# Optimization experiments

Hardware: AMD Instinct MI355X
Metric: run time of the kernel (lower is better)

## Reference

```python
import jax, jax.numpy as jnp
import numpy as np

B, S, H = 2, 2048, 4096
NH, NKV, HD = 32, 8, 128
Q_SIZE, KV_SIZE = NH * HD, NKV * HD
ROPE_THETA = 10000.0


def setup_inputs() -> dict:
    key = jax.random.key(0)
    k1, k2, k3 = jax.random.split(key, 3)
    positions = jnp.tile(jnp.arange(S, dtype=jnp.int64 if jax.config.jax_enable_x64 else jnp.int32), (B, 1))
    hidden_states = jax.random.normal(k1, (B, S, H), dtype=jnp.float32)
    w_qkv = jax.random.normal(k2, (H, Q_SIZE + 2 * KV_SIZE), dtype=jnp.float32) * 0.02
    w_o = jax.random.normal(k3, (Q_SIZE, H), dtype=jnp.float32) * 0.02
    return {"positions": positions, "hidden_states": hidden_states, "w_qkv": w_qkv, "w_o": w_o}


def _apply_rope(x, positions):
    # x: [B, S, nheads, HD]; neox-style rotate-half RoPE
    half = HD // 2
    inv_freq = 1.0 / (ROPE_THETA ** (jnp.arange(0, half, dtype=jnp.float32) / half))
    freqs = positions.astype(jnp.float32)[..., None] * inv_freq  # [B, S, HD/2]
    cos = jnp.cos(freqs)[:, :, None, :]  # [B, S, 1, HD/2]
    sin = jnp.sin(freqs)[:, :, None, :]
    x1, x2 = x[..., :half], x[..., half:]
    return jnp.concatenate([x1 * cos - x2 * sin, x2 * cos + x1 * sin], axis=-1)


def reference(positions, hidden_states, w_qkv, w_o):
    qkv = jnp.einsum("bsh,hd->bsd", hidden_states, w_qkv)
    q = qkv[..., :Q_SIZE].reshape(B, S, NH, HD)
    k = qkv[..., Q_SIZE:Q_SIZE + KV_SIZE].reshape(B, S, NKV, HD)
    v = qkv[..., Q_SIZE + KV_SIZE:].reshape(B, S, NKV, HD)

    q = _apply_rope(q, positions)
    k = _apply_rope(k, positions)

    # GQA: expand kv heads to match query heads
    rep = NH // NKV
    k = jnp.repeat(k, rep, axis=2)  # [B, S, NH, HD]
    v = jnp.repeat(v, rep, axis=2)

    scale = 1.0 / jnp.sqrt(jnp.float32(HD))
    scores = jnp.einsum("bqhd,bkhd->bhqk", q, k) * scale  # [B, NH, S, S]
    causal = jnp.tril(jnp.ones((S, S), dtype=bool))
    scores = jnp.where(causal[None, None], scores, jnp.finfo(scores.dtype).min)
    probs = jax.nn.softmax(scores, axis=-1)

    attn = jnp.einsum("bhqk,bkhd->bqhd", probs, v).reshape(B, S, Q_SIZE)
    return jnp.einsum("bsd,dh->bsh", attn, w_o)
```

## Files before the change

### kernel.cpp

```cpp
#include <hip/hip_runtime.h>
#include <hip/hip_bf16.h>
#include <math.h>


typedef __attribute__((ext_vector_type(8))) __bf16 bf16x8;
typedef __attribute__((ext_vector_type(4))) float floatx4;

__device__ __forceinline__ floatx4 mfma16(bf16x8 a, bf16x8 b, floatx4 c) {
    return __builtin_amdgcn_mfma_f32_16x16x32_bf16(a, b, c, 0, 0, 0);
}

__device__ __forceinline__ void load_lds16(const __hip_bfloat16* g,
                                           __hip_bfloat16* lds_base_uniform) {
    __builtin_amdgcn_global_load_lds(
        (const __attribute__((address_space(1))) unsigned int*)g,
        (__attribute__((address_space(3))) unsigned int*)lds_base_uniform,
        16, 0, 0);
}

__global__ __launch_bounds__(256)
void convert_kernel(const float* __restrict__ in, __hip_bfloat16* __restrict__ out,
                    int n) {
    int i = (blockIdx.x * 256 + threadIdx.x) * 4;
    if (i >= n) return;
    float4 v = *(const float4*)(in + i);
    union { __hip_bfloat16 h[4]; uint2 u; } pk;
    pk.h[0] = __float2bfloat16(v.x);
    pk.h[1] = __float2bfloat16(v.y);
    pk.h[2] = __float2bfloat16(v.z);
    pk.h[3] = __float2bfloat16(v.w);
    *(uint2*)(out + i) = pk.u;
}

__global__ __launch_bounds__(256)
void transpose_f32_bf16_kernel(const float* __restrict__ in,
                               __hip_bfloat16* __restrict__ out, int R, int C) {
    __shared__ __hip_bfloat16 tile[64][65];
    const int r0 = blockIdx.y * 64, c0 = blockIdx.x * 64;
    const int t = threadIdx.x;
    #pragma unroll
    for (int i = 0; i < 16; ++i) {
        int idx = t + 256 * i;
        int rl = idx >> 6, cl = idx & 63;
        tile[rl][cl] = __float2bfloat16(in[(size_t)(r0 + rl) * C + (c0 + cl)]);
    }
    __syncthreads();
    #pragma unroll
    for (int i = 0; i < 16; ++i) {
        int idx = t + 256 * i;
        int cl = idx >> 6, rl = idx & 63;
        out[(size_t)(c0 + cl) * R + (r0 + rl)] = tile[rl][cl];
    }
}

__global__ __launch_bounds__(256)
void transpose_bf16_kernel(const __hip_bfloat16* __restrict__ in,
                           __hip_bfloat16* __restrict__ out, int R, int C) {
    __shared__ __hip_bfloat16 tile[64][65];
    const int bz = blockIdx.z;
    const __hip_bfloat16* inb  = in  + (size_t)bz * R * C;
    __hip_bfloat16*       outb = out + (size_t)bz * R * C;
    const int r0 = blockIdx.y * 64, c0 = blockIdx.x * 64;
    const int t = threadIdx.x;
    #pragma unroll
    for (int i = 0; i < 16; ++i) {
        int idx = t + 256 * i;
        int rl = idx >> 6, cl = idx & 63;
        tile[rl][cl] = inb[(size_t)(r0 + rl) * C + (c0 + cl)];
    }
    __syncthreads();
    #pragma unroll
    for (int i = 0; i < 16; ++i) {
        int idx = t + 256 * i;
        int cl = idx >> 6, rl = idx & 63;
        outb[(size_t)(c0 + cl) * R + (r0 + rl)] = tile[rl][cl];
    }
}

template <int MODE>
__global__ __launch_bounds__(256)
void gemm_bt_kernel(const __hip_bfloat16* __restrict__ A,
                    const __hip_bfloat16* __restrict__ Bt,
                    float* __restrict__ Cp,
                    __hip_bfloat16* __restrict__ Qr,
                    __hip_bfloat16* __restrict__ Kr,
                    __hip_bfloat16* __restrict__ Vv,
                    int M, int N, int K) {
    __shared__ __align__(16) __hip_bfloat16 As[128 * 32];
    __shared__ __align__(16) __hip_bfloat16 Bs[128 * 32];

    const int m0 = blockIdx.y * 128, n0 = blockIdx.x * 128;
    const int tid  = threadIdx.x;
    const int wave = tid >> 6, lane = tid & 63;
    const int quad = lane >> 4, l16 = lane & 15;
    const int wm = (wave >> 1) * 64, wn = (wave & 1) * 64;

    floatx4 acc[4][4] = {};

    for (int kt = 0; kt < K; kt += 32) {
        #pragma unroll
        for (int i = 0; i < 2; ++i) {
            int idx = tid + 256 * i;
            int row = idx >> 2;
            int kc  = (idx & 3) << 3;
            __hip_bfloat16* dstA = &As[(size_t)(wave * 64 + 256 * i) * 8];
            __hip_bfloat16* dstB = &Bs[(size_t)(wave * 64 + 256 * i) * 8];
            load_lds16(&A [(size_t)(m0 + row) * K + kt + kc], dstA);
            load_lds16(&Bt[(size_t)(n0 + row) * K + kt + kc], dstB);
        }
        __syncthreads();

        bf16x8 af[4], bfv[4];
        #pragma unroll
        for (int i = 0; i < 4; ++i)
            af[i]  = *(const bf16x8*)(&As[(wm + i * 16 + l16) * 32 + quad * 8]);
        #pragma unroll
        for (int j = 0; j < 4; ++j)
            bfv[j] = *(const bf16x8*)(&Bs[(wn + j * 16 + l16) * 32 + quad * 8]);
        #pragma unroll
        for (int i = 0; i < 4; ++i)
            #pragma unroll
            for (int j = 0; j < 4; ++j)
                acc[i][j] = mfma16(af[i], bfv[j], acc[i][j]);
        __syncthreads();
    }

    #pragma unroll
    for (int i = 0; i < 4; ++i) {
        #pragma unroll
        for (int j = 0; j < 4; ++j) {
            int col = n0 + wn + j * 16 + l16;
            #pragma unroll
            for (int r = 0; r < 4; ++r) {
                int row = m0 + wm + i * 16 + quad * 4 + r;
                if (MODE == 0) {
                    Cp[(size_t)row * N + col] = acc[i][j][r];
                } else {
                    __hip_bfloat16 v = __float2bfloat16(acc[i][j][r]);
                    int bb = row >> 11, s = row & 2047;
                    int d  = col & 127;
                    if (col < 4096) {
                        int h = col >> 7;
                        Qr[(((size_t)bb * 32 + h) * 2048 + s) * 128 + d] = v;
                    } else if (col < 5120) {
                        int kvh = (col - 4096) >> 7;
                        Kr[(((size_t)bb * 8 + kvh) * 2048 + s) * 128 + d] = v;
                    } else {
                        int kvh = (col - 5120) >> 7;
                        Vv[(((size_t)bb * 8 + kvh) * 2048 + s) * 128 + d] = v;
                    }
                }
            }
        }
    }
}

__global__ __launch_bounds__(256)
void rope_kernel(__hip_bfloat16* __restrict__ x,
                 const int* __restrict__ positions, int nrows, int bshift) {
    int gid = blockIdx.x * 256 + threadIdx.x;
    if (gid >= nrows * 64) return;
    int row = gid >> 6, d = gid & 63;
    int s = row & 2047;
    int b = row >> bshift;
    float p = (float)positions[(b << 11) + s];
    float ang = p * expf(-0.14391156831212787f * (float)d);
    float sn, cs;
    sincosf(ang, &sn, &cs);
    __hip_bfloat16* ptr = x + (size_t)row * 128;
    float x1 = __bfloat162float(ptr[d]);
    float x2 = __bfloat162float(ptr[d + 64]);
    ptr[d]      = __float2bfloat16(x1 * cs - x2 * sn);
    ptr[d + 64] = __float2bfloat16(x2 * cs + x1 * sn);
}

__global__ __launch_bounds__(256)
void attn_kernel(const __hip_bfloat16* __restrict__ Qr,
                 const __hip_bfloat16* __restrict__ Kr,
                 const __hip_bfloat16* __restrict__ Vt,
                 __hip_bfloat16* __restrict__ Ao) {
    __shared__ __align__(16) __hip_bfloat16 Ks[32 * 136];
    __shared__ __align__(16) __hip_bfloat16 Vs[128 * 36];
    __shared__ __align__(16) __hip_bfloat16 Pl[4][32 * 40];

    const int tid  = threadIdx.x;
    const int wave = tid >> 6, lane = tid & 63;
    const int quad = lane >> 4, l16 = lane & 15;
    const int qb = (gridDim.x - 1) - blockIdx.x;
    const int q0 = qb * 128;
    const int qr0 = q0 + wave * 32;
    const int h  = blockIdx.y;
    const int b  = blockIdx.z;
    const int kv = h >> 2;

    const __hip_bfloat16* Qb = Qr + ((size_t)b * 32 + h)  * 2048 * 128;
    const __hip_bfloat16* Kb = Kr + ((size_t)b * 8  + kv) * 2048 * 128;
    const __hip_bfloat16* Vb = Vt + ((size_t)b * 8  + kv) * 128 * 2048;

    bf16x8 qf[2][4];
    #pragma unroll
    for (int i = 0; i < 2; ++i)
        #pragma unroll
        for (int kc = 0; kc < 4; ++kc)
            qf[i][kc] = *(const bf16x8*)(
                &Qb[(size_t)(qr0 + i * 16 + l16) * 128 + kc * 32 + quad * 8]);

    float m_i[2][4], l_i[2][4];
    #pragma unroll
    for (int i = 0; i < 2; ++i)
        #pragma unroll
        for (int r = 0; r < 4; ++r) { m_i[i][r] = -1e30f; l_i[i][r] = 0.0f; }
    floatx4 o[2][8] = {};

    const float scale = 0.08838834764831845f;
    const int kmax = q0 + 127;

    for (int ks = 0; ks <= kmax; ks += 32) {
        #pragma unroll
        for (int p = 0; p < 2; ++p) {
            int idx = tid + 256 * p;
            int krow = idx >> 4, kcol = (idx & 15) << 3;
            *(uint4*)(&Ks[krow * 136 + kcol]) =
                *(const uint4*)(&Kb[(size_t)(ks + krow) * 128 + kcol]);
        }
        #pragma unroll
        for (int p = 0; p < 2; ++p) {
            int idx = tid + 256 * p;
            int d = idx >> 2, koff = (idx & 3) << 3;
            *(uint4*)(&Vs[d * 36 + koff]) =
                *(const uint4*)(&Vb[(size_t)d * 2048 + ks + koff]);
        }
        __syncthreads();

        if (ks <= qr0 + 31) {
            floatx4 sacc[2][2] = {};
            #pragma unroll
            for (int j = 0; j < 2; ++j) {
                #pragma unroll
                for (int kc = 0; kc < 4; ++kc) {
                    bf16x8 kf = *(const bf16x8*)(
                        &Ks[(j * 16 + l16) * 136 + kc * 32 + quad * 8]);
                    #pragma unroll
                    for (int i = 0; i < 2; ++i)
                        sacc[i][j] = mfma16(qf[i][kc], kf, sacc[i][j]);
                }
            }

            float pv[2][2][4], alpha[2][4];
            #pragma unroll
            for (int i = 0; i < 2; ++i) {
                #pragma unroll
                for (int r = 0; r < 4; ++r) {
                    int row = qr0 + i * 16 + quad * 4 + r;
                    float s0 = sacc[i][0][r] * scale;
                    float s1 = sacc[i][1][r] * scale;
                    if (ks + l16 > row)      s0 = -1e30f;
                    if (ks + 16 + l16 > row) s1 = -1e30f;
                    float mx = fmaxf(s0, s1);
                    #pragma unroll
                    for (int off = 1; off < 16; off <<= 1)
                        mx = fmaxf(mx, __shfl_xor(mx, off, 64));
                    float mnew = fmaxf(m_i[i][r], mx);
                    float a  = __expf(m_i[i][r] - mnew);
                    float p0 = __expf(s0 - mnew);
                    float p1 = __expf(s1 - mnew);
                    float rs = p0 + p1;
                    #pragma unroll
                    for (int off = 1; off < 16; off <<= 1)
                        rs += __shfl_xor(rs, off, 64);
                    l_i[i][r] = l_i[i][r] * a + rs;
                    m_i[i][r] = mnew;
                    alpha[i][r] = a;
                    pv[i][0][r] = p0;
                    pv[i][1][r] = p1;
                }
            }

            #pragma unroll
            for (int i = 0; i < 2; ++i)
                #pragma unroll
                for (int dn = 0; dn < 8; ++dn)
                    #pragma unroll
                    for (int r = 0; r < 4; ++r)
                        o[i][dn][r] *= alpha[i][r];

            #pragma unroll
            for (int i = 0; i < 2; ++i)
                #pragma unroll
                for (int j = 0; j < 2; ++j)
                    #pragma unroll
                    for (int r = 0; r < 4; ++r)
                        Pl[wave][(i * 16 + quad * 4 + r) * 40 + j * 16 + l16] =
                            __float2bfloat16(pv[i][j][r]);

            bf16x8 pf[2];
            #pragma unroll
            for (int i = 0; i < 2; ++i)
                pf[i] = *(const bf16x8*)(&Pl[wave][(i * 16 + l16) * 40 + quad * 8]);

            #pragma unroll
            for (int dn = 0; dn < 8; ++dn) {
                bf16x8 vf = *(const bf16x8*)(
                    &Vs[(dn * 16 + l16) * 36 + quad * 8]);
                #pragma unroll
                for (int i = 0; i < 2; ++i)
                    o[i][dn] = mfma16(pf[i], vf, o[i][dn]);
            }
        }
        __syncthreads();
    }

    #pragma unroll
    for (int i = 0; i < 2; ++i) {
        #pragma unroll
        for (int r = 0; r < 4; ++r) {
            float inv = 1.0f / l_i[i][r];
            int row = qr0 + i * 16 + quad * 4 + r;
            size_t base = ((size_t)b * 2048 + row) * 4096 + (size_t)h * 128;
            #pragma unroll
            for (int dn = 0; dn < 8; ++dn)
                Ao[base + dn * 16 + l16] = __float2bfloat16(o[i][dn][r] * inv);
        }
    }
}

extern "C" void kernel_launch(void* const* d_in, const int* in_sizes, int n_in,
                              void* d_out, int out_size, void* d_ws, size_t ws_size,
                              hipStream_t stream) {
    const int*   positions = (const int*)d_in[0];
    const float* hidden    = (const float*)d_in[1];
    const float* wqkv      = (const float*)d_in[2];
    const float* wo        = (const float*)d_in[3];
    float* out = (float*)d_out;

    __hip_bfloat16* WqkvT = (__hip_bfloat16*)d_ws;
    __hip_bfloat16* WoT   = WqkvT + 25165824;
    __hip_bfloat16* Hb    = WoT   + 16777216;
    __hip_bfloat16* Qr    = Hb    + 16777216;
    __hip_bfloat16* Kr    = Qr    + 16777216;
    __hip_bfloat16* Vv    = Kr    + 4194304;
    __hip_bfloat16* Ao    = WqkvT;
    __hip_bfloat16* Vt    = Hb;

    convert_kernel<<<16777216 / 1024, 256, 0, stream>>>(hidden, Hb, 16777216);
    transpose_f32_bf16_kernel<<<dim3(6144 / 64, 4096 / 64), 256, 0, stream>>>(
        wqkv, WqkvT, 4096, 6144);
    transpose_f32_bf16_kernel<<<dim3(4096 / 64, 4096 / 64), 256, 0, stream>>>(
        wo, WoT, 4096, 4096);

    gemm_bt_kernel<1><<<dim3(6144 / 128, 4096 / 128), 256, 0, stream>>>(
        Hb, WqkvT, nullptr, Qr, Kr, Vv, 4096, 6144, 4096);

    rope_kernel<<<(131072 * 64) / 256, 256, 0, stream>>>(Qr, positions, 131072, 16);
    rope_kernel<<<(32768  * 64) / 256, 256, 0, stream>>>(Kr, positions, 32768, 14);

    transpose_bf16_kernel<<<dim3(128 / 64, 2048 / 64, 16), 256, 0, stream>>>(
        Vv, Vt, 2048, 128);

    attn_kernel<<<dim3(2048 / 128, 32, 2), 256, 0, stream>>>(Qr, Kr, Vt, Ao);

    gemm_bt_kernel<0><<<dim3(4096 / 128, 4096 / 128), 256, 0, stream>>>(
        Ao, WoT, out, nullptr, nullptr, nullptr, 4096, 4096, 4096);
}
```

Baseline: 1.222 ms.

## Double KV tile to 64 and prefetch next tile into registers during softmax

The attention kernel now processes 64 keys per iteration instead of 32, which halves the number of barrier-synchronised iterations. It prefetches the next K/V tile from global memory into registers while the current tile's softmax runs, so load latency overlaps compute. It also writes probabilities straight to LDS inside the softmax loop, raises wave priority around the MFMA blocks, and sets a minimum-occupancy launch bound. The trade-off is higher register and LDS use per block, plus more wasted work on partially masked diagonal tiles.

```diff
diff --git a/kernel.cpp b/kernel.cpp
--- a/kernel.cpp
+++ b/kernel.cpp
@@ -174,14 +174,14 @@
     ptr[d + 64] = __float2bfloat16(x2 * cs + x1 * sn);
 }
 
-__global__ __launch_bounds__(256)
+__global__ __launch_bounds__(256, 3)
 void attn_kernel(const __hip_bfloat16* __restrict__ Qr,
                  const __hip_bfloat16* __restrict__ Kr,
                  const __hip_bfloat16* __restrict__ Vt,
                  __hip_bfloat16* __restrict__ Ao) {
-    __shared__ __align__(16) __hip_bfloat16 Ks[32 * 136];
-    __shared__ __align__(16) __hip_bfloat16 Vs[128 * 36];
-    __shared__ __align__(16) __hip_bfloat16 Pl[4][32 * 40];
+    __shared__ __align__(16) __hip_bfloat16 Ks[64 * 132];
+    __shared__ __align__(16) __hip_bfloat16 Vs[128 * 68];
+    __shared__ __align__(16) __hip_bfloat16 Pl[4][32 * 68];
 
     const int tid  = threadIdx.x;
     const int wave = tid >> 6, lane = tid & 63;
@@ -197,6 +197,9 @@
     const __hip_bfloat16* Kb = Kr + ((size_t)b * 8  + kv) * 2048 * 128;
     const __hip_bfloat16* Vb = Vt + ((size_t)b * 8  + kv) * 128 * 2048;
 
+    const int krow = tid >> 4,            kcol = (tid & 15) << 3;
+    const int vrow = tid >> 3,            vcol = (tid & 7)  << 3;
+
     bf16x8 qf[2][4];
     #pragma unroll
     for (int i = 0; i < 2; ++i)
@@ -215,67 +218,88 @@
     const float scale = 0.08838834764831845f;
     const int kmax = q0 + 127;
 
-    for (int ks = 0; ks <= kmax; ks += 32) {
-        #pragma unroll
-        for (int p = 0; p < 2; ++p) {
-            int idx = tid + 256 * p;
-            int krow = idx >> 4, kcol = (idx & 15) << 3;
-            *(uint4*)(&Ks[krow * 136 + kcol]) =
-                *(const uint4*)(&Kb[(size_t)(ks + krow) * 128 + kcol]);
-        }
-        #pragma unroll
-        for (int p = 0; p < 2; ++p) {
-            int idx = tid + 256 * p;
-            int d = idx >> 2, koff = (idx & 3) << 3;
-            *(uint4*)(&Vs[d * 36 + koff]) =
-                *(const uint4*)(&Vb[(size_t)d * 2048 + ks + koff]);
+    uint4 kreg[4], vreg[4];
+    #pragma unroll
+    for (int p = 0; p < 4; ++p) {
+        kreg[p] = *(const uint4*)(&Kb[(size_t)(krow + 16 * p) * 128 + kcol]);
+        vreg[p] = *(const uint4*)(&Vb[(size_t)(vrow + 32 * p) * 2048 + vcol]);
+    }
+
+    for (int ks = 0; ks <= kmax; ks += 64) {
+        #pragma unroll
+        for (int p = 0; p < 4; ++p) {
+            *(uint4*)(&Ks[(krow + 16 * p) * 132 + kcol]) = kreg[p];
+            *(uint4*)(&Vs[(vrow + 32 * p) * 68  + vcol]) = vreg[p];
         }
         __syncthreads();
 
-        if (ks <= qr0 + 31) {
-            floatx4 sacc[2][2] = {};
-            #pragma unroll
-            for (int j = 0; j < 2; ++j) {
-                #pragma unroll
-                for (int kc = 0; kc < 4; ++kc) {
-                    bf16x8 kf = *(const bf16x8*)(
-                        &Ks[(j * 16 + l16) * 136 + kc * 32 + quad * 8]);
-                    #pragma unroll
-                    for (int i = 0; i < 2; ++i)
-                        sacc[i][j] = mfma16(qf[i][kc], kf, sacc[i][j]);
-                }
-            }
-
-            float pv[2][2][4], alpha[2][4];
+        const bool live = (ks <= qr0 + 31);
+        float alpha[2][4];
+
+        if (live) {
+            floatx4 sacc[2][4] = {};
+            __builtin_amdgcn_s_setprio(1);
+            #pragma unroll
+            for (int kc = 0; kc < 4; ++kc) {
+                bf16x8 kf[4];
+                #pragma unroll
+                for (int j = 0; j < 4; ++j)
+                    kf[j] = *(const bf16x8*)(
+                        &Ks[(j * 16 + l16) * 132 + kc * 32 + quad * 8]);
+                #pragma unroll
+                for (int i = 0; i < 2; ++i)
+                    #pragma unroll
+                    for (int j = 0; j < 4; ++j)
+                        sacc[i][j] = mfma16(qf[i][kc], kf[j], sacc[i][j]);
+            }
+            __builtin_amdgcn_s_setprio(0);
+
             #pragma unroll
             for (int i = 0; i < 2; ++i) {
                 #pragma unroll
                 for (int r = 0; r < 4; ++r) {
                     int row = qr0 + i * 16 + quad * 4 + r;
-                    float s0 = sacc[i][0][r] * scale;
-                    float s1 = sacc[i][1][r] * scale;
-                    if (ks + l16 > row)      s0 = -1e30f;
-                    if (ks + 16 + l16 > row) s1 = -1e30f;
-                    float mx = fmaxf(s0, s1);
+                    float s[4];
+                    #pragma unroll
+                    for (int j = 0; j < 4; ++j) {
+                        s[j] = sacc[i][j][r] * scale;
+                        if (ks + j * 16 + l16 > row) s[j] = -1e30f;
+                    }
+                    float mx = fmaxf(fmaxf(s[0], s[1]), fmaxf(s[2], s[3]));
                     #pragma unroll
                     for (int off = 1; off < 16; off <<= 1)
                         mx = fmaxf(mx, __shfl_xor(mx, off, 64));
                     float mnew = fmaxf(m_i[i][r], mx);
                     float a  = __expf(m_i[i][r] - mnew);
-                    float p0 = __expf(s0 - mnew);
-                    float p1 = __expf(s1 - mnew);
-                    float rs = p0 + p1;
+                    float rs = 0.0f;
+                    #pragma unroll
+                    for (int j = 0; j < 4; ++j) {
+                        float p = __expf(s[j] - mnew);
+                        rs += p;
+                        Pl[wave][(i * 16 + quad * 4 + r) * 68 + j * 16 + l16] =
+                            __float2bfloat16(p);
+                    }
                     #pragma unroll
                     for (int off = 1; off < 16; off <<= 1)
                         rs += __shfl_xor(rs, off, 64);
                     l_i[i][r] = l_i[i][r] * a + rs;
                     m_i[i][r] = mnew;
                     alpha[i][r] = a;
-                    pv[i][0][r] = p0;
-                    pv[i][1][r] = p1;
                 }
             }
-
+        }
+
+        if (ks + 64 <= kmax) {
+            #pragma unroll
+            for (int p = 0; p < 4; ++p) {
+                kreg[p] = *(const uint4*)(
+                    &Kb[(size_t)(ks + 64 + krow + 16 * p) * 128 + kcol]);
+                vreg[p] = *(const uint4*)(
+                    &Vb[(size_t)(vrow + 32 * p) * 2048 + ks + 64 + vcol]);
+            }
+        }
+
+        if (live) {
             #pragma unroll
             for (int i = 0; i < 2; ++i)
                 #pragma unroll
@@ -284,28 +308,27 @@
                     for (int r = 0; r < 4; ++r)
                         o[i][dn][r] *= alpha[i][r];
 
+            bf16x8 pf[2][2];
             #pragma unroll
             for (int i = 0; i < 2; ++i)
                 #pragma unroll
-                for (int j = 0; j < 2; ++j)
-                    #pragma unroll
-                    for (int r = 0; r < 4; ++r)
-                        Pl[wave][(i * 16 + quad * 4 + r) * 40 + j * 16 + l16] =
-                            __float2bfloat16(pv[i][j][r]);
-
-            bf16x8 pf[2];
-            #pragma unroll
-            for (int i = 0; i < 2; ++i)
-                pf[i] = *(const bf16x8*)(&Pl[wave][(i * 16 + l16) * 40 + quad * 8]);
-
+                for (int k2 = 0; k2 < 2; ++k2)
+                    pf[i][k2] = *(const bf16x8*)(
+                        &Pl[wave][(i * 16 + l16) * 68 + k2 * 32 + quad * 8]);
+
+            __builtin_amdgcn_s_setprio(1);
             #pragma unroll
             for (int dn = 0; dn < 8; ++dn) {
-                bf16x8 vf = *(const bf16x8*)(
-                    &Vs[(dn * 16 + l16) * 36 + quad * 8]);
-                #pragma unroll
-                for (int i = 0; i < 2; ++i)
-                    o[i][dn] = mfma16(pf[i], vf, o[i][dn]);
-            }
+                #pragma unroll
+                for (int k2 = 0; k2 < 2; ++k2) {
+                    bf16x8 vf = *(const bf16x8*)(
+                        &Vs[(dn * 16 + l16) * 68 + k2 * 32 + quad * 8]);
+                    #pragma unroll
+                    for (int i = 0; i < 2; ++i)
+                        o[i][dn] = mfma16(pf[i][k2], vf, o[i][dn]);
+                }
+            }
+            __builtin_amdgcn_s_setprio(0);
         }
         __syncthreads();
     }
```

Measured after the change: 1.447 ms. 1.18x slower.

## Fold softmax scale into Q RoPE, compute row sums via MFMA, skip masks on full tiles

Applied to the files above, without the earlier changes.

The attention scale is now applied to Q inside the RoPE kernel, which removes the per-score multiply. Row sums are accumulated with an MFMA against a vector of ones instead of a cross-lane shuffle reduction. The causal mask is skipped on tiles that lie entirely below the diagonal, and s_setprio raises wave priority around the MFMA blocks. The tradeoffs are extra MFMA work, bf16 rounding of P entering the denominator (which now matches the numerator), and Q being pre-scaled before its bf16 rounding.

```diff
diff --git a/kernel.cpp b/kernel.cpp
--- a/kernel.cpp
+++ b/kernel.cpp
@@ -157,7 +157,8 @@
 
 __global__ __launch_bounds__(256)
 void rope_kernel(__hip_bfloat16* __restrict__ x,
-                 const int* __restrict__ positions, int nrows, int bshift) {
+                 const int* __restrict__ positions, int nrows, int bshift,
+                 float qscale) {
     int gid = blockIdx.x * 256 + threadIdx.x;
     if (gid >= nrows * 64) return;
     int row = gid >> 6, d = gid & 63;
@@ -170,8 +171,8 @@
     __hip_bfloat16* ptr = x + (size_t)row * 128;
     float x1 = __bfloat162float(ptr[d]);
     float x2 = __bfloat162float(ptr[d + 64]);
-    ptr[d]      = __float2bfloat16(x1 * cs - x2 * sn);
-    ptr[d + 64] = __float2bfloat16(x2 * cs + x1 * sn);
+    ptr[d]      = __float2bfloat16((x1 * cs - x2 * sn) * qscale);
+    ptr[d + 64] = __float2bfloat16((x2 * cs + x1 * sn) * qscale);
 }
 
 __global__ __launch_bounds__(256)
@@ -205,14 +206,18 @@
             qf[i][kc] = *(const bf16x8*)(
                 &Qb[(size_t)(qr0 + i * 16 + l16) * 128 + kc * 32 + quad * 8]);
 
-    float m_i[2][4], l_i[2][4];
+    float m_i[2][4];
     #pragma unroll
     for (int i = 0; i < 2; ++i)
         #pragma unroll
-        for (int r = 0; r < 4; ++r) { m_i[i][r] = -1e30f; l_i[i][r] = 0.0f; }
+        for (int r = 0; r < 4; ++r) m_i[i][r] = -1e30f;
     floatx4 o[2][8] = {};
-
-    const float scale = 0.08838834764831845f;
+    floatx4 lsum[2] = {};
+
+    bf16x8 ones;
+    #pragma unroll
+    for (int e = 0; e < 8; ++e) ones[e] = (__bf16)1.0f;
+
     const int kmax = q0 + 127;
 
     for (int ks = 0; ks <= kmax; ks += 32) {
@@ -233,7 +238,10 @@
         __syncthreads();
 
         if (ks <= qr0 + 31) {
+            const bool fullt = (ks + 31 <= qr0);
+
             floatx4 sacc[2][2] = {};
+            __builtin_amdgcn_s_setprio(1);
             #pragma unroll
             for (int j = 0; j < 2; ++j) {
                 #pragma unroll
@@ -245,17 +253,19 @@
                         sacc[i][j] = mfma16(qf[i][kc], kf, sacc[i][j]);
                 }
             }
-
-            float pv[2][2][4], alpha[2][4];
+            __builtin_amdgcn_s_setprio(0);
+
             #pragma unroll
             for (int i = 0; i < 2; ++i) {
                 #pragma unroll
                 for (int r = 0; r < 4; ++r) {
                     int row = qr0 + i * 16 + quad * 4 + r;
-                    float s0 = sacc[i][0][r] * scale;
-                    float s1 = sacc[i][1][r] * scale;
-                    if (ks + l16 > row)      s0 = -1e30f;
-                    if (ks + 16 + l16 > row) s1 = -1e30f;
+                    float s0 = sacc[i][0][r];
+                    float s1 = sacc[i][1][r];
+                    if (!fullt) {
+                        if (ks + l16 > row)      s0 = -1e30f;
+                        if (ks + 16 + l16 > row) s1 = -1e30f;
+                    }
                     float mx = fmaxf(s0, s1);
                     #pragma unroll
                     for (int off = 1; off < 16; off <<= 1)
@@ -264,40 +274,27 @@
                     float a  = __expf(m_i[i][r] - mnew);
                     float p0 = __expf(s0 - mnew);
                     float p1 = __expf(s1 - mnew);
-                    float rs = p0 + p1;
+                    Pl[wave][(i * 16 + quad * 4 + r) * 40 + l16]      =
+                        __float2bfloat16(p0);
+                    Pl[wave][(i * 16 + quad * 4 + r) * 40 + 16 + l16] =
+                        __float2bfloat16(p1);
+                    m_i[i][r] = mnew;
+                    lsum[i][r] *= a;
                     #pragma unroll
-                    for (int off = 1; off < 16; off <<= 1)
-                        rs += __shfl_xor(rs, off, 64);
-                    l_i[i][r] = l_i[i][r] * a + rs;
-                    m_i[i][r] = mnew;
-                    alpha[i][r] = a;
-                    pv[i][0][r] = p0;
-                    pv[i][1][r] = p1;
+                    for (int dn = 0; dn < 8; ++dn)
+                        o[i][dn][r] *= a;
                 }
             }
 
-            #pragma unroll
-            for (int i = 0; i < 2; ++i)
-                #pragma unroll
-                for (int dn = 0; dn < 8; ++dn)
-                    #pragma unroll
-                    for (int r = 0; r < 4; ++r)
-                        o[i][dn][r] *= alpha[i][r];
-
-            #pragma unroll
-            for (int i = 0; i < 2; ++i)
-                #pragma unroll
-                for (int j = 0; j < 2; ++j)
-                    #pragma unroll
-                    for (int r = 0; r < 4; ++r)
-                        Pl[wave][(i * 16 + quad * 4 + r) * 40 + j * 16 + l16] =
-                            __float2bfloat16(pv[i][j][r]);
-
             bf16x8 pf[2];
             #pragma unroll
             for (int i = 0; i < 2; ++i)
                 pf[i] = *(const bf16x8*)(&Pl[wave][(i * 16 + l16) * 40 + quad * 8]);
 
+            __builtin_amdgcn_s_setprio(1);
+            #pragma unroll
+            for (int i = 0; i < 2; ++i)
+                lsum[i] = mfma16(pf[i], ones, lsum[i]);
             #pragma unroll
             for (int dn = 0; dn < 8; ++dn) {
                 bf16x8 vf = *(const bf16x8*)(
@@ -306,6 +303,7 @@
                 for (int i = 0; i < 2; ++i)
                     o[i][dn] = mfma16(pf[i], vf, o[i][dn]);
             }
+            __builtin_amdgcn_s_setprio(0);
         }
         __syncthreads();
     }
@@ -314,7 +312,7 @@
     for (int i = 0; i < 2; ++i) {
         #pragma unroll
         for (int r = 0; r < 4; ++r) {
-            float inv = 1.0f / l_i[i][r];
+            float inv = 1.0f / lsum[i][r];
             int row = qr0 + i * 16 + quad * 4 + r;
             size_t base = ((size_t)b * 2048 + row) * 4096 + (size_t)h * 128;
             #pragma unroll
@@ -351,8 +349,10 @@
     gemm_bt_kernel<1><<<dim3(6144 / 128, 4096 / 128), 256, 0, stream>>>(
         Hb, WqkvT, nullptr, Qr, Kr, Vv, 4096, 6144, 4096);
 
-    rope_kernel<<<(131072 * 64) / 256, 256, 0, stream>>>(Qr, positions, 131072, 16);
-    rope_kernel<<<(32768  * 64) / 256, 256, 0, stream>>>(Kr, positions, 32768, 14);
+    rope_kernel<<<(131072 * 64) / 256, 256, 0, stream>>>(
+        Qr, positions, 131072, 16, 0.08838834764831845f);
+    rope_kernel<<<(32768  * 64) / 256, 256, 0, stream>>>(
+        Kr, positions, 32768, 14, 1.0f);
 
     transpose_bf16_kernel<<<dim3(128 / 64, 2048 / 64, 16), 256, 0, stream>>>(
         Vv, Vt, 2048, 128);
```

Result: faster. 1.082 ms (-11.5%).
